# Performance work log

Hardware: AMD Instinct MI355X
Metric: run time of the kernel (lower is better)

The kernel has to match this reference:

```python
import jax, jax.numpy as jnp
import numpy as np

SW, FB, EMB, H = 96, 64, 512, 3   # seg_width, freq_bandwidth, embedding_dim, num_heads
B, T = 4, 1024
F = SW * FB


def setup_inputs() -> dict:
    key = jax.random.key(0)
    ks = jax.random.split(key, 12)
    s = 0.02
    dh = SW // H
    return {
        "x": jax.random.normal(ks[0], (B, T, F), jnp.float32),
        "o_enc": jax.random.randint(ks[1], (B, T), 0, 2, jnp.int32),
        "r_enc": jax.random.normal(ks[2], (B, T, EMB), jnp.float32),
        "Wq": jax.random.normal(ks[3], (SW, SW), jnp.float32) * s,
        "bq": jnp.zeros((SW,), jnp.float32),
        "Wk": jax.random.normal(ks[4], (SW, SW), jnp.float32) * s,
        "bk": jnp.zeros((SW,), jnp.float32),
        "Wv": jax.random.normal(ks[5], (SW, SW), jnp.float32) * s,
        "bv": jnp.zeros((SW,), jnp.float32),
        "Er": jax.random.normal(ks[6], (FB, dh), jnp.float32) * s,   # relative pos embeddings, max_len = FB
        "W1": jax.random.normal(ks[7], (SW, 4 * SW), jnp.float32) * s,
        "b1": jnp.zeros((4 * SW,), jnp.float32),
        "W2": jax.random.normal(ks[8], (4 * SW, SW), jnp.float32) * s,
        "b2": jnp.zeros((SW,), jnp.float32),
        "We": jax.random.normal(ks[9], (F, EMB), jnp.float32) * s,
        "be": jnp.zeros((EMB,), jnp.float32),
    }


def _skew(qer):
    # qer: (N, h, L, L) -> Srel via Music-Transformer skewing
    padded = jnp.pad(qer, ((0, 0), (0, 0), (0, 0), (1, 0)))      # (N,h,L,L+1)
    n, h, l, l1 = padded.shape
    return padded.reshape(n, h, l1, l)[:, :, 1:, :]               # (N,h,L,L)


def _rel_attention(x, Wq, bq, Wk, bk, Wv, bv, Er):
    # x: (N, L, D); relative global self-attention with causal mask
    N, L, D = x.shape
    dh = D // H

    def heads(t):
        return t.reshape(N, L, H, dh).transpose(0, 2, 1, 3)       # (N,h,L,dh)

    q = heads(x @ Wq + bq)
    k = heads(x @ Wk + bk)
    v = heads(x @ Wv + bv)
    qer = jnp.einsum('nhld,md->nhlm', q, Er)                      # (N,h,L,L)
    srel = _skew(qer)
    scores = (jnp.einsum('nhld,nhmd->nhlm', q, k) + srel) / jnp.sqrt(jnp.asarray(dh, x.dtype))
    causal = jnp.triu(jnp.ones((L, L), bool), 1)
    scores = jnp.where(causal, jnp.finfo(scores.dtype).min, scores)
    attn = jax.nn.softmax(scores, axis=-1)
    out = jnp.einsum('nhlm,nhmd->nhld', attn, v)
    return out.transpose(0, 2, 1, 3).reshape(N, L, D)


def _segmentwise_mean(data, block_ids):
    # data: (B,T,E), block_ids: (B,T) contiguous non-decreasing segment ids in [0,T)
    Bn, Tn, En = data.shape
    seg_sum = jax.vmap(lambda d, i: jax.ops.segment_sum(d, i, num_segments=Tn))(data, block_ids)
    cnt = jax.vmap(lambda i: jax.ops.segment_sum(jnp.ones_like(i), i, num_segments=Tn))(block_ids)
    means = seg_sum / jnp.maximum(cnt, 1).astype(data.dtype)[..., None]
    is_start = jnp.concatenate(
        [jnp.ones((Bn, 1), bool), block_ids[:, 1:] != block_ids[:, :-1]], axis=1)
    gathered = jnp.take_along_axis(means, block_ids[..., None], axis=1)   # (B,T,E)
    # original writes each block's mean only at the block's first position, zeros elsewhere
    return jnp.where(is_start[..., None], gathered, jnp.zeros((), data.dtype))


def reference(x, o_enc, r_enc, Wq, bq, Wk, bk, Wv, bv, Er, W1, b1, W2, b2, We, be):
    Bn, Tn, Fn = x.shape
    xr = x.reshape(Bn * Tn, SW, FB).transpose(0, 2, 1)            # (B*T, FB, SW)
    emb = _rel_attention(xr, Wq, bq, Wk, bk, Wv, bv, Er)
    emb = jax.nn.relu(emb @ W1 + b1) @ W2 + b2                    # FFN: SW -> 4SW -> SW
    emb = emb.transpose(0, 2, 1).reshape(Bn, Tn, Fn)
    emb = emb @ We + be                                           # (B,T,EMB)
    # nn.LayerNorm(emb.shape): normalize over the WHOLE tensor, no affine, eps=1e-8
    mu = emb.mean()
    var = ((emb - mu) ** 2).mean()
    emb = (emb - mu) / jnp.sqrt(var + 1e-8)
    # _regionalize: block ids from cumsum of binary boundary indicators
    block_ids = jnp.cumsum(o_enc, axis=1)
    block_ids = block_ids - block_ids[:, :1]                      # matches 'if b[0]==1: b -= 1'
    block_means = _segmentwise_mean(emb, block_ids)
    return block_means + r_enc + emb
```

## Files before the change

kernel.cpp:

```cpp
#include <hip/hip_runtime.h>
#include <hip/hip_bf16.h>


typedef __attribute__((ext_vector_type(8))) short bf16x8;
typedef __attribute__((ext_vector_type(4))) float f32x4;

struct PtrTab { const void* p[16]; };

enum : int {
  O_WQT = 0,
  O_BQ  = 9984,
  O_WKT = 10080,
  O_BK  = 20064,
  O_WVT = 20160,
  O_BV  = 30144,
  O_ER  = 30240,
  O_W1T = 32288,
  O_B1  = 72224,
  O_W2C = 72608,
  O_B2  = 118688,
  O_WET = 118784
};

__device__ __forceinline__ float b2f(__hip_bfloat16 v) { return __bfloat162float(v); }
__device__ __forceinline__ __hip_bfloat16 f2b(float v) { return __float2bfloat16(v); }

__global__ __launch_bounds__(256) void prep_kernel(PtrTab tab,
                                                   __hip_bfloat16* __restrict__ Wc,
                                                   float* __restrict__ sums)
{
    __shared__ __hip_bfloat16 tile[64][65];
    const int bid = blockIdx.x, tid = threadIdx.x;
    const int kt = bid % 96, nt = bid / 96;
    const float* We = (const float*)tab.p[14];
    const int k0 = kt * 64, n0 = nt * 64;
    for (int e = tid; e < 4096; e += 256) {
        int kk = e >> 6, nn = e & 63;
        tile[nn][kk] = f2b(We[(size_t)(k0 + kk) * 512 + n0 + nn]);
    }
    __syncthreads();
    __hip_bfloat16* dstT = Wc + O_WET + ((size_t)nt * 96 + kt) * 4096;
    for (int e = tid; e < 4096; e += 256) dstT[e] = tile[e >> 6][e & 63];

    const int g = bid * 256 + tid;
    const int stride = gridDim.x * 256;
    const float* Wq = (const float*)tab.p[3];
    const float* bq = (const float*)tab.p[4];
    const float* Wk = (const float*)tab.p[5];
    const float* bk = (const float*)tab.p[6];
    const float* Wv = (const float*)tab.p[7];
    const float* bv = (const float*)tab.p[8];
    const float* Er = (const float*)tab.p[9];
    const float* W1 = (const float*)tab.p[10];
    const float* b1 = (const float*)tab.p[11];
    const float* W2 = (const float*)tab.p[12];
    const float* b2 = (const float*)tab.p[13];

    for (int t = 0; t < 3; ++t) {
        const float* W = (t == 0 ? Wq : t == 1 ? Wk : Wv);
        __hip_bfloat16* d = Wc + t * 10080;
        for (int i = g; i < 9984; i += stride) {
            int j = i / 104, c = i - j * 104;
            d[i] = (c < 96) ? f2b(W[c * 96 + j]) : f2b(0.0f);
        }
    }
    for (int i = g; i < 96; i += stride) {
        Wc[O_BQ + i] = f2b(bq[i]);
        Wc[O_BK + i] = f2b(bk[i]);
        Wc[O_BV + i] = f2b(bv[i]);
        Wc[O_B2 + i] = f2b(b2[i]);
    }
    for (int i = g; i < 2048; i += stride) Wc[O_ER + i] = f2b(Er[i]);
    for (int i = g; i < 39936; i += stride) {
        int j = i / 104, c = i - j * 104;
        Wc[O_W1T + i] = (c < 96) ? f2b(W1[c * 384 + j]) : f2b(0.0f);
    }
    for (int i = g; i < 384; i += stride) Wc[O_B1 + i] = f2b(b1[i]);
    for (int i = g; i < 46080; i += stride) {
        int kc = i / 3840, r = i - kc * 3840;
        int nn = r / 40, kk = r - nn * 40;
        Wc[O_W2C + i] = (kk < 32) ? f2b(W2[(kc * 32 + kk) * 96 + nn]) : f2b(0.0f);
    }
    if (g < 2) sums[g] = 0.f;
}

__global__ __launch_bounds__(256, 4) void attn_ffn_kernel(
    const float* __restrict__ x, const __hip_bfloat16* __restrict__ Wc,
    __hip_bfloat16* __restrict__ M)
{
    const int n = blockIdx.x, tid = threadIdx.x;
    const int w = tid >> 6, lane = tid & 63, quad = lane >> 4, ln = lane & 15;

    __shared__ __align__(16) char smem[40448];
    __hip_bfloat16* xs  = (__hip_bfloat16*)(smem);
    __hip_bfloat16* wb  = (__hip_bfloat16*)(smem);
    __hip_bfloat16* kS  = (__hip_bfloat16*)(smem + 13312);
    __hip_bfloat16* vT  = (__hip_bfloat16*)(smem + 26624);
    __hip_bfloat16* hid = (__hip_bfloat16*)(smem + 13312);

    const f32x4 z4 = {0.f, 0.f, 0.f, 0.f};
    const int rowb = 16 * w + quad * 4;

    bf16x8 wf[9], wfn[9];
    #pragma unroll
    for (int i = 0; i < 9; ++i)
        wf[i] = *(const bf16x8*)(Wc + O_WQT + ((i % 3) * 16 + ln) * 104 + (i / 3) * 32 + quad * 8);

    {
        const float* xb = x + (size_t)n * 6144;
        const int sb = w * 24;
        for (int c = 0; c < 3; ++c) {
            float v[8];
            #pragma unroll
            for (int j = 0; j < 8; ++j) v[j] = xb[(sb + c * 8 + j) * 64 + lane];
            union { __hip_bfloat16 h[8]; bf16x8 v8; } pk;
            #pragma unroll
            for (int j = 0; j < 8; ++j) pk.h[j] = f2b(v[j]);
            *(bf16x8*)(xs + lane * 104 + sb + c * 8) = pk.v8;
        }
    }
    __syncthreads();

    bf16x8 af[3];
    #pragma unroll
    for (int ks = 0; ks < 3; ++ks)
        af[ks] = *(const bf16x8*)(xs + (16 * w + ln) * 104 + ks * 32 + quad * 8);

    bf16x8 aqr[3];

    for (int st = 0; st < 6; ++st) {
        const int t = st >> 1, half = st & 1;
        if (st < 5) {
            const __hip_bfloat16* nb = Wc + ((st + 1) >> 1) * 10080 + ((st + 1) & 1) * 4992;
            #pragma unroll
            for (int i = 0; i < 9; ++i)
                wfn[i] = *(const bf16x8*)(nb + ((i % 3) * 16 + ln) * 104 + (i / 3) * 32 + quad * 8);
        }
        f32x4 acc[3] = {z4, z4, z4};
        #pragma unroll
        for (int ks = 0; ks < 3; ++ks)
            #pragma unroll
            for (int ct = 0; ct < 3; ++ct)
                acc[ct] = __builtin_amdgcn_mfma_f32_16x16x32_bf16(af[ks], wf[ks * 3 + ct], acc[ct], 0, 0, 0);
        const int j0 = half * 48;
        const __hip_bfloat16* bt = Wc + 9984 + t * 10080;
        #pragma unroll
        for (int ct = 0; ct < 3; ++ct) {
            int col = j0 + ct * 16 + ln;
            float bb = b2f(bt[col]);
            if (t < 2) {
                #pragma unroll
                for (int r = 0; r < 4; ++r)
                    kS[(rowb + r) * 104 + col] = f2b(acc[ct][r] + bb);
            } else {
                union { __hip_bfloat16 h4[4]; uint2 u; } pk;
                #pragma unroll
                for (int r = 0; r < 4; ++r) pk.h4[r] = f2b(acc[ct][r] + bb);
                *(uint2*)(vT + col * 72 + rowb) = pk.u;
            }
        }
        if (t == 0 && half == 1) {
            #pragma unroll
            for (int h = 0; h < 3; ++h)
                aqr[h] = *(const bf16x8*)(kS + (16 * w + ln) * 104 + h * 32 + quad * 8);
        }
        #pragma unroll
        for (int i = 0; i < 9; ++i) wf[i] = wfn[i];
    }

    bf16x8 erf[4];
    #pragma unroll
    for (int tn = 0; tn < 4; ++tn)
        erf[tn] = *(const bf16x8*)(Wc + O_ER + (16 * tn + ln) * 32 + quad * 8);
    __syncthreads();

    bf16x8 pf0, pf1, pf2;
    {
        const bf16x8* src = (const bf16x8*)(Wc + O_W1T);
        pf0 = src[tid]; pf1 = src[tid + 256];
        if (tid + 512 < 624) pf2 = src[tid + 512];
    }

    __hip_bfloat16* S2 = xs + 32;
    const int ql = 16 * w + ln;
    const int sshift = 63 - ql;
    f32x4 oacc[3][2] = {{z4, z4}, {z4, z4}, {z4, z4}};

    #pragma unroll
    for (int h = 0; h < 3; ++h) {
        const int c0 = h * 32;
        bf16x8 aq = aqr[h];
        #pragma unroll
        for (int tn = 0; tn < 4; ++tn) {
            f32x4 q4 = __builtin_amdgcn_mfma_f32_16x16x32_bf16(erf[tn], aq, z4, 0, 0, 0);
            #pragma unroll
            for (int r = 0; r < 4; ++r) {
                int e = 16 * tn + 4 * quad + r;
                if (e >= sshift) S2[ql * 104 + (e - sshift)] = f2b(q4[r]);
            }
        }
        float sco[4][4];
        #pragma unroll
        for (int tn = 0; tn < 4; ++tn) {
            bf16x8 kf = *(const bf16x8*)(kS + (16 * tn + ln) * 104 + c0 + quad * 8);
            f32x4 s1 = __builtin_amdgcn_mfma_f32_16x16x32_bf16(kf, aq, z4, 0, 0, 0);
            #pragma unroll
            for (int r = 0; r < 4; ++r) sco[tn][r] = s1[r];
        }
        #pragma unroll
        for (int tn = 0; tn < 4; ++tn) {
            union { __hip_bfloat16 h4[4]; uint2 u; } sr;
            sr.u = *(const uint2*)(S2 + ql * 104 + 16 * tn + 4 * quad);
            #pragma unroll
            for (int r = 0; r < 4; ++r) {
                int m = 16 * tn + 4 * quad + r;
                sco[tn][r] = (m <= ql)
                    ? (sco[tn][r] + b2f(sr.h4[r])) * 0.17677669529663687f
                    : -3.0e38f;
            }
        }
        float mt[4];
        #pragma unroll
        for (int tn = 0; tn < 4; ++tn)
            mt[tn] = fmaxf(fmaxf(sco[tn][0], sco[tn][1]), fmaxf(sco[tn][2], sco[tn][3]));
        float mx = fmaxf(fmaxf(mt[0], mt[1]), fmaxf(mt[2], mt[3]));
        mx = fmaxf(mx, __shfl_xor(mx, 16, 64));
        mx = fmaxf(mx, __shfl_xor(mx, 32, 64));
        float st_[4];
        #pragma unroll
        for (int tn = 0; tn < 4; ++tn) {
            #pragma unroll
            for (int r = 0; r < 4; ++r) sco[tn][r] = __expf(sco[tn][r] - mx);
            st_[tn] = (sco[tn][0] + sco[tn][1]) + (sco[tn][2] + sco[tn][3]);
        }
        float sum = (st_[0] + st_[1]) + (st_[2] + st_[3]);
        sum += __shfl_xor(sum, 16, 64);
        sum += __shfl_xor(sum, 32, 64);
        const float inv = 1.0f / sum;
        #pragma unroll
        for (int tn = 0; tn < 4; ++tn) {
            union { __hip_bfloat16 h4[4]; uint2 u; } pk;
            #pragma unroll
            for (int r = 0; r < 4; ++r) pk.h4[r] = f2b(sco[tn][r] * inv);
            *(uint2*)(S2 + ql * 104 + 16 * tn + 4 * quad) = pk.u;
        }
        #pragma unroll
        for (int ks2 = 0; ks2 < 2; ++ks2) {
            bf16x8 pa = *(const bf16x8*)(S2 + ql * 104 + ks2 * 32 + quad * 8);
            #pragma unroll
            for (int t2 = 0; t2 < 2; ++t2) {
                bf16x8 vb = *(const bf16x8*)(vT + (c0 + 16 * t2 + ln) * 72 + ks2 * 32 + quad * 8);
                oacc[h][t2] = __builtin_amdgcn_mfma_f32_16x16x32_bf16(pa, vb, oacc[h][t2], 0, 0, 0);
            }
        }
    }
    #pragma unroll
    for (int h = 0; h < 3; ++h)
        #pragma unroll
        for (int t2 = 0; t2 < 2; ++t2)
            #pragma unroll
            for (int r = 0; r < 4; ++r)
                xs[(rowb + r) * 104 + h * 32 + 16 * t2 + ln] = f2b(oacc[h][t2][r]);

    bf16x8 cf[3];
    #pragma unroll
    for (int ks = 0; ks < 3; ++ks)
        cf[ks] = *(const bf16x8*)(xs + (16 * w + ln) * 104 + ks * 32 + quad * 8);

    f32x4 acc2[6] = {z4, z4, z4, z4, z4, z4};
    bf16x8 w2f[6], w2fn[6];
    for (int jh = 0; jh < 2; ++jh) {
        for (int cc = 0; cc < 4; ++cc) {
            const int j0g = jh * 192 + cc * 48;
            __syncthreads();
            {
                bf16x8* dst = (bf16x8*)wb;
                dst[tid] = pf0;
                dst[tid + 256] = pf1;
                if (tid + 512 < 624) dst[tid + 512] = pf2;
                if (cc < 3) {
                    const bf16x8* src = (const bf16x8*)(Wc + O_W1T + jh * 19968 + (cc + 1) * 4992);
                    pf0 = src[tid]; pf1 = src[tid + 256];
                    if (tid + 512 < 624) pf2 = src[tid + 512];
                } else {
                    const __hip_bfloat16* nb = Wc + O_W2C + (jh * 6) * 3840;
                    #pragma unroll
                    for (int ct = 0; ct < 6; ++ct)
                        w2f[ct] = *(const bf16x8*)(nb + (ct * 16 + ln) * 40 + quad * 8);
                }
            }
            __syncthreads();
            f32x4 a1[3] = {z4, z4, z4};
            #pragma unroll
            for (int ks = 0; ks < 3; ++ks) {
                #pragma unroll
                for (int ct = 0; ct < 3; ++ct) {
                    bf16x8 b = *(const bf16x8*)(wb + (ct * 16 + ln) * 104 + ks * 32 + quad * 8);
                    a1[ct] = __builtin_amdgcn_mfma_f32_16x16x32_bf16(cf[ks], b, a1[ct], 0, 0, 0);
                }
            }
            #pragma unroll
            for (int ct = 0; ct < 3; ++ct) {
                int colg = j0g + ct * 16 + ln;
                int coll = cc * 48 + ct * 16 + ln;
                float bb = b2f(Wc[O_B1 + colg]);
                #pragma unroll
                for (int r = 0; r < 4; ++r)
                    hid[(rowb + r) * 200 + coll] = f2b(fmaxf(a1[ct][r] + bb, 0.f));
            }
        }
        for (int kc = 0; kc < 6; ++kc) {
            if (kc < 5) {
                const __hip_bfloat16* nb = Wc + O_W2C + (jh * 6 + kc + 1) * 3840;
                #pragma unroll
                for (int ct = 0; ct < 6; ++ct)
                    w2fn[ct] = *(const bf16x8*)(nb + (ct * 16 + ln) * 40 + quad * 8);
            } else if (jh == 0) {
                const bf16x8* src = (const bf16x8*)(Wc + O_W1T + 19968);
                pf0 = src[tid]; pf1 = src[tid + 256];
                if (tid + 512 < 624) pf2 = src[tid + 512];
            }
            bf16x8 a = *(const bf16x8*)(hid + (16 * w + ln) * 200 + kc * 32 + quad * 8);
            #pragma unroll
            for (int ct = 0; ct < 6; ++ct)
                acc2[ct] = __builtin_amdgcn_mfma_f32_16x16x32_bf16(a, w2f[ct], acc2[ct], 0, 0, 0);
            if (kc < 5) {
                #pragma unroll
                for (int ct = 0; ct < 6; ++ct) w2f[ct] = w2fn[ct];
            }
        }
    }

    __hip_bfloat16* Mg = M + (size_t)n * 6144;
    #pragma unroll
    for (int ct = 0; ct < 6; ++ct) {
        int d = ct * 16 + ln;
        float bb = b2f(Wc[O_B2 + d]);
        union { __hip_bfloat16 h4[4]; uint2 u; } pk;
        #pragma unroll
        for (int r = 0; r < 4; ++r) pk.h4[r] = f2b(acc2[ct][r] + bb);
        *(uint2*)((char*)Mg + (size_t)(d * 64 + rowb) * 2) = pk.u;
    }
}

__global__ __launch_bounds__(256) void gemm_kernel(
    const __hip_bfloat16* __restrict__ A,
    const __hip_bfloat16* __restrict__ Wc,
    const float* __restrict__ be,
    float* __restrict__ Y,
    float* __restrict__ sums)
{
    __shared__ __align__(16) __hip_bfloat16 As[2][64 * 72];
    __shared__ __align__(16) __hip_bfloat16 Bs[2][64 * 72];
    const int row0 = blockIdx.x * 64, nt = blockIdx.y, col0 = nt * 64;
    const int tid = threadIdx.x;
    const int w = tid >> 6, lane = tid & 63, quad = lane >> 4, ln = lane & 15;
    const int r0 = tid >> 3, c0_ = (tid & 7) * 8;
    const int r1 = r0 + 32,  c1_ = c0_;
    const size_t abase0 = (size_t)(row0 + r0) * 6144 + c0_;
    const size_t abase1 = (size_t)(row0 + r1) * 6144 + c1_;
    const __hip_bfloat16* Bsrc = Wc + O_WET + (size_t)nt * 96 * 4096;
    const size_t bbase0 = (size_t)r0 * 64 + c0_;
    const size_t bbase1 = (size_t)r1 * 64 + c1_;

    const f32x4 z4 = {0.f, 0.f, 0.f, 0.f};
    f32x4 acc[4] = {z4, z4, z4, z4};

    bf16x8 pa0 = *(const bf16x8*)(A + abase0);
    bf16x8 pa1 = *(const bf16x8*)(A + abase1);
    bf16x8 pb0 = *(const bf16x8*)(Bsrc + bbase0);
    bf16x8 pb1 = *(const bf16x8*)(Bsrc + bbase1);
    *(bf16x8*)(&As[0][r0 * 72 + c0_]) = pa0;
    *(bf16x8*)(&As[0][r1 * 72 + c1_]) = pa1;
    *(bf16x8*)(&Bs[0][r0 * 72 + c0_]) = pb0;
    *(bf16x8*)(&Bs[0][r1 * 72 + c1_]) = pb1;
    __syncthreads();

    for (int kt = 0; kt < 96; ++kt) {
        const int cur = kt & 1;
        if (kt < 95) {
            pa0 = *(const bf16x8*)(A + abase0 + (kt + 1) * 64);
            pa1 = *(const bf16x8*)(A + abase1 + (kt + 1) * 64);
            pb0 = *(const bf16x8*)(Bsrc + (size_t)(kt + 1) * 4096 + bbase0);
            pb1 = *(const bf16x8*)(Bsrc + (size_t)(kt + 1) * 4096 + bbase1);
        }
        #pragma unroll
        for (int ks = 0; ks < 2; ++ks) {
            bf16x8 a = *(const bf16x8*)(&As[cur][(16 * w + ln) * 72 + ks * 32 + quad * 8]);
            #pragma unroll
            for (int tn = 0; tn < 4; ++tn) {
                bf16x8 b = *(const bf16x8*)(&Bs[cur][(16 * tn + ln) * 72 + ks * 32 + quad * 8]);
                acc[tn] = __builtin_amdgcn_mfma_f32_16x16x32_bf16(a, b, acc[tn], 0, 0, 0);
            }
        }
        if (kt < 95) {
            *(bf16x8*)(&As[cur ^ 1][r0 * 72 + c0_]) = pa0;
            *(bf16x8*)(&As[cur ^ 1][r1 * 72 + c1_]) = pa1;
            *(bf16x8*)(&Bs[cur ^ 1][r0 * 72 + c0_]) = pb0;
            *(bf16x8*)(&Bs[cur ^ 1][r1 * 72 + c1_]) = pb1;
        }
        __syncthreads();
    }
    float s = 0.f, s2 = 0.f;
    #pragma unroll
    for (int tn = 0; tn < 4; ++tn) {
        int col = col0 + 16 * tn + ln;
        float bb = be[col];
        #pragma unroll
        for (int r = 0; r < 4; ++r) {
            float v = acc[tn][r] + bb;
            Y[(size_t)(row0 + 16 * w + quad * 4 + r) * 512 + col] = v;
            s += v; s2 += v * v;
        }
    }
    #pragma unroll
    for (int off = 1; off < 64; off <<= 1) {
        s  += __shfl_xor(s, off, 64);
        s2 += __shfl_xor(s2, off, 64);
    }
    __shared__ float r1s[4], r2s[4];
    if (lane == 0) { r1s[w] = s; r2s[w] = s2; }
    __syncthreads();
    if (tid == 0) {
        atomicAdd(&sums[0], r1s[0] + r1s[1] + r1s[2] + r1s[3]);
        atomicAdd(&sums[1], r2s[0] + r2s[1] + r2s[2] + r2s[3]);
    }
}

__global__ __launch_bounds__(256) void segid_kernel(const int* __restrict__ o_enc,
                                                    int* __restrict__ bids) {
    __shared__ int ts[256];
    const int b = blockIdx.x, tid = threadIdx.x;
    const int* o = o_enc + b * 1024;
    int v0 = o[4 * tid], v1 = o[4 * tid + 1], v2 = o[4 * tid + 2], v3 = o[4 * tid + 3];
    int p0 = v0, p1 = p0 + v1, p2 = p1 + v2, p3 = p2 + v3;
    ts[tid] = p3;
    __syncthreads();
    for (int off = 1; off < 256; off <<= 1) {
        int mine = ts[tid];
        int add = (tid >= off) ? ts[tid - off] : 0;
        __syncthreads();
        ts[tid] = mine + add;
        __syncthreads();
    }
    const int excl = (tid > 0) ? ts[tid - 1] : 0;
    const int off0 = o[0];
    int* bid = bids + b * 1024;
    bid[4 * tid]     = excl + p0 - off0;
    bid[4 * tid + 1] = excl + p1 - off0;
    bid[4 * tid + 2] = excl + p2 - off0;
    bid[4 * tid + 3] = excl + p3 - off0;
}

__global__ __launch_bounds__(256) void final_kernel(
    const float* __restrict__ Y, const int* __restrict__ bids,
    const float* __restrict__ sums, const float* __restrict__ r_enc,
    float* __restrict__ out)
{
    const int bt = blockIdx.x;
    const int b = bt >> 10, t = bt & 1023;
    const float mu = sums[0] * (1.0f / 2097152.0f);
    const float var = sums[1] * (1.0f / 2097152.0f) - mu * mu;
    const float rstd = rsqrtf(var + 1e-8f);
    const int* bid = bids + b * 1024;
    const int my = bid[t];
    const bool is_start = (t == 0) || (bid[t - 1] != my);
    int t2 = t + 1;
    float invc = 0.f;
    if (is_start) {
        while (t2 < 1024 && bid[t2] == my) ++t2;
        invc = 1.0f / (float)(t2 - t);
    }
    for (int e = threadIdx.x; e < 512; e += 256) {
        const size_t base = (size_t)bt * 512 + e;
        float res = (Y[base] - mu) * rstd + r_enc[base];
        if (is_start) {
            float s = 0.f;
            for (int tt = t; tt < t2; ++tt)
                s += (Y[((size_t)(b * 1024 + tt)) * 512 + e] - mu) * rstd;
            res += s * invc;
        }
        out[base] = res;
    }
}

extern "C" void kernel_launch(void* const* d_in, const int* in_sizes, int n_in,
                              void* d_out, int out_size, void* d_ws, size_t ws_size,
                              hipStream_t stream) {
    PtrTab tab;
    for (int i = 0; i < 16; ++i) tab.p[i] = d_in[i];

    char* ws = (char*)d_ws;
    __hip_bfloat16* M  = (__hip_bfloat16*)ws;
    float* Y           = (float*)(ws + 50331648);
    float* sums        = (float*)(ws + 58720256);
    int*   bids        = (int*)(ws + 58720320);
    __hip_bfloat16* Wc = (__hip_bfloat16*)(ws + 58736768);

    prep_kernel<<<768, 256, 0, stream>>>(tab, Wc, sums);
    attn_ffn_kernel<<<4096, 256, 0, stream>>>((const float*)d_in[0], Wc, M);
    gemm_kernel<<<dim3(64, 8), 256, 0, stream>>>(M, Wc, (const float*)d_in[15], Y, sums);
    segid_kernel<<<4, 256, 0, stream>>>((const int*)d_in[1], bids);
    final_kernel<<<4096, 256, 0, stream>>>(Y, bids, sums, (const float*)d_in[2], (float*)d_out);
}
```

Before: 382.5 us.

## Use direct global-to-LDS loads with XOR swizzle and K=128 tiles in embedding GEMM

Rewrites the embedding GEMM's operand staging to use global_load_lds (direct global-to-shared copies), removing the register round-trip and the explicit LDS stores. The padded LDS layout is replaced by an XOR-swizzled layout to avoid bank conflicts, and the K tile is doubled to 128 so the loop runs half as many iterations and hits half as many barriers. In exchange, LDS use grows to 64 KB per block, which may reduce occupancy. Correctness also depends on the asynchronous LDS writes finishing before the barrier, since no explicit vmcnt wait is added.

```diff
diff --git a/kernel.cpp b/kernel.cpp
--- a/kernel.cpp
+++ b/kernel.cpp
@@ -24,6 +24,12 @@
 
 __device__ __forceinline__ float b2f(__hip_bfloat16 v) { return __bfloat162float(v); }
 __device__ __forceinline__ __hip_bfloat16 f2b(float v) { return __float2bfloat16(v); }
+
+__device__ __forceinline__ void gload16(const void* g, void* l) {
+    __builtin_amdgcn_global_load_lds(
+        (const __attribute__((address_space(1))) void*)g,
+        (__attribute__((address_space(3))) void*)l, 16, 0, 0);
+}
 
 __global__ __launch_bounds__(256) void prep_kernel(PtrTab tab,
                                                    __hip_bfloat16* __restrict__ Wc,
@@ -350,57 +356,53 @@
     float* __restrict__ Y,
     float* __restrict__ sums)
 {
-    __shared__ __align__(16) __hip_bfloat16 As[2][64 * 72];
-    __shared__ __align__(16) __hip_bfloat16 Bs[2][64 * 72];
+    __shared__ __align__(16) char gsm[65536];
     const int row0 = blockIdx.x * 64, nt = blockIdx.y, col0 = nt * 64;
     const int tid = threadIdx.x;
     const int w = tid >> 6, lane = tid & 63, quad = lane >> 4, ln = lane & 15;
-    const int r0 = tid >> 3, c0_ = (tid & 7) * 8;
-    const int r1 = r0 + 32,  c1_ = c0_;
-    const size_t abase0 = (size_t)(row0 + r0) * 6144 + c0_;
-    const size_t abase1 = (size_t)(row0 + r1) * 6144 + c1_;
     const __hip_bfloat16* Bsrc = Wc + O_WET + (size_t)nt * 96 * 4096;
-    const size_t bbase0 = (size_t)r0 * 64 + c0_;
-    const size_t bbase1 = (size_t)r1 * 64 + c1_;
 
     const f32x4 z4 = {0.f, 0.f, 0.f, 0.f};
     f32x4 acc[4] = {z4, z4, z4, z4};
 
-    bf16x8 pa0 = *(const bf16x8*)(A + abase0);
-    bf16x8 pa1 = *(const bf16x8*)(A + abase1);
-    bf16x8 pb0 = *(const bf16x8*)(Bsrc + bbase0);
-    bf16x8 pb1 = *(const bf16x8*)(Bsrc + bbase1);
-    *(bf16x8*)(&As[0][r0 * 72 + c0_]) = pa0;
-    *(bf16x8*)(&As[0][r1 * 72 + c1_]) = pa1;
-    *(bf16x8*)(&Bs[0][r0 * 72 + c0_]) = pb0;
-    *(bf16x8*)(&Bs[0][r1 * 72 + c1_]) = pb1;
+    auto stage = [&](int buf, int kt) {
+        char* Ab = gsm + buf * 16384;
+        char* Bb = gsm + 32768 + buf * 16384;
+        #pragma unroll
+        for (int j = 0; j < 4; ++j) {
+            const int b = j * 4096 + tid * 16;
+            const int row = b >> 8;
+            const int s = b ^ ((row & 7) << 4);
+            const int col = (s & 255) >> 1;
+            gload16(A + (size_t)(row0 + row) * 6144 + kt * 128 + col,
+                    Ab + j * 4096 + w * 1024);
+            gload16(Bsrc + (size_t)(2 * kt + (col >> 6)) * 4096 + row * 64 + (col & 63),
+                    Bb + j * 4096 + w * 1024);
+        }
+    };
+
+    stage(0, 0);
     __syncthreads();
 
-    for (int kt = 0; kt < 96; ++kt) {
+    for (int kt = 0; kt < 48; ++kt) {
         const int cur = kt & 1;
-        if (kt < 95) {
-            pa0 = *(const bf16x8*)(A + abase0 + (kt + 1) * 64);
-            pa1 = *(const bf16x8*)(A + abase1 + (kt + 1) * 64);
-            pb0 = *(const bf16x8*)(Bsrc + (size_t)(kt + 1) * 4096 + bbase0);
-            pb1 = *(const bf16x8*)(Bsrc + (size_t)(kt + 1) * 4096 + bbase1);
-        }
-        #pragma unroll
-        for (int ks = 0; ks < 2; ++ks) {
-            bf16x8 a = *(const bf16x8*)(&As[cur][(16 * w + ln) * 72 + ks * 32 + quad * 8]);
+        if (kt < 47) stage(cur ^ 1, kt + 1);
+        const char* Ab = gsm + cur * 16384;
+        const char* Bb = gsm + 32768 + cur * 16384;
+        #pragma unroll
+        for (int ks = 0; ks < 4; ++ks) {
+            const int ra = ((16 * w + ln) << 8) + ks * 64 + quad * 16;
+            bf16x8 a = *(const bf16x8*)(Ab + (ra ^ ((ln & 7) << 4)));
             #pragma unroll
             for (int tn = 0; tn < 4; ++tn) {
-                bf16x8 b = *(const bf16x8*)(&Bs[cur][(16 * tn + ln) * 72 + ks * 32 + quad * 8]);
+                const int rb = ((16 * tn + ln) << 8) + ks * 64 + quad * 16;
+                bf16x8 b = *(const bf16x8*)(Bb + (rb ^ ((ln & 7) << 4)));
                 acc[tn] = __builtin_amdgcn_mfma_f32_16x16x32_bf16(a, b, acc[tn], 0, 0, 0);
             }
         }
-        if (kt < 95) {
-            *(bf16x8*)(&As[cur ^ 1][r0 * 72 + c0_]) = pa0;
-            *(bf16x8*)(&As[cur ^ 1][r1 * 72 + c1_]) = pa1;
-            *(bf16x8*)(&Bs[cur ^ 1][r0 * 72 + c0_]) = pb0;
-            *(bf16x8*)(&Bs[cur ^ 1][r1 * 72 + c1_]) = pb1;
-        }
         __syncthreads();
     }
+
     float s = 0.f, s2 = 0.f;
     #pragma unroll
     for (int tn = 0; tn < 4; ++tn) {
@@ -418,7 +420,8 @@
         s  += __shfl_xor(s, off, 64);
         s2 += __shfl_xor(s2, off, 64);
     }
-    __shared__ float r1s[4], r2s[4];
+    float* r1s = (float*)gsm;
+    float* r2s = r1s + 4;
     if (lane == 0) { r1s[w] = s; r2s[w] = s2; }
     __syncthreads();
     if (tid == 0) {
```

New measurement: 374.2 us. 2.2% less time.
